# Kernel optimization log

Hardware: AMD Instinct MI355X
Metric: run time of the kernel (lower is better)

## Reference

```python
import jax, jax.numpy as jnp
import numpy as np

N = 50000   # num_nodes
E = 800000  # num_edges (avg degree 16)
D = 128     # input_dim
H = 128     # hidden_dim
EPS = 1e-5


def _linear_params(key, fan_in, fan_out):
    k1, k2 = jax.random.split(key)
    s = 1.0 / np.sqrt(fan_in)
    W = jax.random.uniform(k1, (fan_in, fan_out), jnp.float32, -s, s)
    b = jax.random.uniform(k2, (fan_out,), jnp.float32, -s, s)
    return W, b


def setup_inputs() -> dict:
    key = jax.random.key(0)
    ks = jax.random.split(key, 10)
    x = jax.random.normal(ks[0], (N, D), jnp.float32)
    edge_index = jax.random.randint(ks[1], (2, E), 0, N)
    edge_weight = jax.random.uniform(ks[2], (E,), jnp.float32)
    W1, b1 = _linear_params(ks[3], D, H)
    W2, b2 = _linear_params(ks[4], H, H)
    W3, b3 = _linear_params(ks[5], H, H)
    Wh, bh = _linear_params(ks[6], H, H)
    Wa, ba = _linear_params(ks[7], H, 1)
    Wz, bz = _linear_params(ks[8], H, 1)
    ones = jnp.ones((H,), jnp.float32)
    zeros = jnp.zeros((H,), jnp.float32)
    return dict(x=x, edge_index=edge_index, edge_weight=edge_weight,
                W1=W1, b1=b1, W2=W2, b2=b2, W3=W3, b3=b3,
                g1=ones, be1=zeros, g2=ones, be2=zeros, g3=ones, be3=zeros,
                Wh=Wh, bh=bh, Wa=Wa, ba=ba, Wz=Wz, bz=bz)


def _batchnorm(h, g, b):
    mu = jnp.mean(h, axis=0)
    var = jnp.mean((h - mu) ** 2, axis=0)  # biased, as torch BN training
    return (h - mu) * jax.lax.rsqrt(var + EPS) * g + b


def reference(x, edge_index, edge_weight,
              W1, b1, W2, b2, W3, b3,
              g1, be1, g2, be2, g3, be3,
              Wh, bh, Wa, ba, Wz, bz):
    row, col = edge_index[0], edge_index[1]
    loop = jnp.arange(N)
    row_f = jnp.concatenate([row, loop])   # sources (with self-loops)
    col_f = jnp.concatenate([col, loop])   # targets
    w_f = jnp.concatenate([edge_weight, jnp.ones((N,), edge_weight.dtype)])
    deg = jax.ops.segment_sum(w_f, col_f, num_segments=N)
    dinv = jnp.where(deg > 0, jax.lax.rsqrt(deg), 0.0)
    norm = dinv[row_f] * w_f * dinv[col_f]  # [E+N]

    def conv(h, W, b):
        hw = h @ W  # [N,H]
        msg = hw[row_f] * norm[:, None]  # gather + scale
        return jax.ops.segment_sum(msg, col_f, num_segments=N) + b  # scatter-add

    h = jax.nn.relu(_batchnorm(conv(x, W1, b1), g1, be1))
    h = jax.nn.relu(_batchnorm(conv(h, W2, b2), g2, be2))
    h = jax.nn.relu(_batchnorm(conv(h, W3, b3), g3, be3))
    # dropout is identity in eval
    h = jax.nn.relu(h @ Wh + bh)
    ace = h[0] @ Wa + ba  # target_indices[0]
    h2 = h[1] @ Wz + bz   # target_indices[1]
    return jnp.concatenate([ace, h2], axis=0)  # [2]
```

## Files before the change

### kernel.cpp

```cpp
#include <hip/hip_runtime.h>


typedef unsigned short u16;
typedef unsigned int u32;
typedef unsigned long long u64;
typedef short bf16x8 __attribute__((ext_vector_type(8)));
typedef float f32x4 __attribute__((ext_vector_type(4)));

#define NREP 64

__device__ inline float bf2f(u16 u) { return __uint_as_float(((u32)u) << 16); }
__device__ inline u16 f2bf(float f) {
  u32 u = __float_as_uint(f);
  return (u16)((u + 0x7FFFu + ((u >> 16) & 1u)) >> 16);
}

__global__ __launch_bounds__(256) void k_zero_cnt(int* cnt, int n) {
  int i = blockIdx.x * 256 + threadIdx.x;
  if (i < n) cnt[i] = 0;
}

__global__ __launch_bounds__(256) void k_count_rank(const int* __restrict__ col,
                                                    int* __restrict__ cnt,
                                                    int* __restrict__ rank, int e) {
  int i = blockIdx.x * 256 + threadIdx.x;
  if (i < e) rank[i] = atomicAdd(&cnt[col[i]], 1);
}

__global__ __launch_bounds__(256) void k_scan1(const int* __restrict__ cnt,
                                               int* __restrict__ ptr,
                                               int* __restrict__ bsum, int n) {
  __shared__ int sh[256];
  int t = threadIdx.x;
  int i = blockIdx.x * 256 + t;
  int v = (i < n) ? cnt[i] : 0;
  sh[t] = v;
  __syncthreads();
  for (int d = 1; d < 256; d <<= 1) {
    int u = (t >= d) ? sh[t - d] : 0;
    __syncthreads();
    sh[t] += u;
    __syncthreads();
  }
  if (i < n) ptr[i] = sh[t] - v;
  if (t == 255) bsum[blockIdx.x] = sh[255];
}

__global__ __launch_bounds__(256) void k_scan2(int* __restrict__ bsum, int nb) {
  __shared__ int sh[256];
  int t = threadIdx.x;
  int v = (t < nb) ? bsum[t] : 0;
  sh[t] = v;
  __syncthreads();
  for (int d = 1; d < 256; d <<= 1) {
    int u = (t >= d) ? sh[t - d] : 0;
    __syncthreads();
    sh[t] += u;
    __syncthreads();
  }
  if (t < nb) bsum[t] = sh[t] - v;
}

__global__ __launch_bounds__(256) void k_scan3(int* __restrict__ ptr,
                                               const int* __restrict__ bsum,
                                               int n, int e) {
  int i = blockIdx.x * 256 + threadIdx.x;
  if (i < n) ptr[i] += bsum[blockIdx.x];
  if (i == 0) ptr[n] = e;
}

__global__ __launch_bounds__(256) void k_fill(const int* __restrict__ row,
                                              const int* __restrict__ col,
                                              const float* __restrict__ w,
                                              const int* __restrict__ ptr,
                                              const int* __restrict__ rank,
                                              int2* __restrict__ emeta, int e) {
  int i = blockIdx.x * 256 + threadIdx.x;
  if (i < e) {
    int pos = ptr[col[i]] + rank[i];
    emeta[pos] = make_int2(row[i] << 8, __float_as_int(w[i]));
  }
}

__global__ __launch_bounds__(256) void k_deg_dinv(const int* __restrict__ ptr,
                                                  const int2* __restrict__ emeta,
                                                  float* __restrict__ dinv, int n) {
  int i = blockIdx.x * 256 + threadIdx.x;
  if (i >= n) return;
  int j = ptr[i], end = ptr[i + 1];
  float d = 1.0f;
  for (; j < end; ++j) d += __int_as_float(emeta[j].y);
  dinv[i] = rsqrtf(d);
}

__global__ __launch_bounds__(256) void k_coef(const int* __restrict__ ptr,
                                              int2* __restrict__ emeta,
                                              const float* __restrict__ dinv, int n) {
  int i = blockIdx.x * 256 + threadIdx.x;
  if (i >= n) return;
  float dc = dinv[i];
  int j = ptr[i], end = ptr[i + 1];
  for (; j < end; ++j) {
    int2 m = emeta[j];
    emeta[j] = make_int2(m.x,
        __float_as_int(dinv[m.x >> 8] * __int_as_float(m.y) * dc));
  }
}

__global__ __launch_bounds__(256) void k_wpack(const float* __restrict__ W0,
                                               const float* __restrict__ W1,
                                               const float* __restrict__ W2,
                                               u64* __restrict__ cells) {
  const float* W = (blockIdx.x == 0) ? W0 : (blockIdx.x == 1) ? W1 : W2;
  u64* out = cells + (size_t)blockIdx.x * 4096;
  int t = threadIdx.x;
#pragma unroll
  for (int i = 0; i < 16; ++i) {
    int cell = t + 256 * i;
    int col = cell >> 5;
    int k4 = cell & 31;
    int k = k4 * 4;
    u64 c = (u64)f2bf(W[(size_t)(k + 0) * 128 + col]) |
            ((u64)f2bf(W[(size_t)(k + 1) * 128 + col]) << 16) |
            ((u64)f2bf(W[(size_t)(k + 2) * 128 + col]) << 32) |
            ((u64)f2bf(W[(size_t)(k + 3) * 128 + col]) << 48);
    out[col * 32 + (k4 ^ (col & 15))] = c;
  }
}

__global__ __launch_bounds__(256) void k_gemm(const void* __restrict__ Ain,
                                              int a_is_f32,
                                              const u64* __restrict__ Wc,
                                              u16* __restrict__ C,
                                              const float* __restrict__ ab,
                                              float* __restrict__ Szero,
                                              int n) {
  __shared__ u64 As64[128 * 32];
  __shared__ u64 Ws64[128 * 32];
  __shared__ float absh[256];
  int t = threadIdx.x;
  if (blockIdx.x < 16) {
#pragma unroll
    for (int i = 0; i < 4; ++i)
      Szero[blockIdx.x * 1024 + t + 256 * i] = 0.f;
  }
  {
    const ulonglong2* src = (const ulonglong2*)Wc;
    ulonglong2* dst = (ulonglong2*)Ws64;
#pragma unroll
    for (int i = 0; i < 8; ++i) dst[t + 256 * i] = src[t + 256 * i];
  }
  if (ab) {
    if (t < 128) {
      absh[t] = ab[t];
      absh[128 + t] = ab[128 + t];
    }
  }

  int row0 = blockIdx.x * 128;
  int nr = min(128, n - row0);

  if (a_is_f32) {
    const float4* src = (const float4*)((const float*)Ain + (size_t)row0 * 128);
#pragma unroll
    for (int i = 0; i < 16; ++i) {
      int idx = t + 256 * i;
      int r = idx >> 5;
      int j4 = idx & 31;
      float4 v = (r < nr) ? src[idx] : make_float4(0.f, 0.f, 0.f, 0.f);
      u64 cell = (u64)f2bf(v.x) | ((u64)f2bf(v.y) << 16) |
                 ((u64)f2bf(v.z) << 32) | ((u64)f2bf(v.w) << 48);
      As64[r * 32 + (j4 ^ (r & 15))] = cell;
    }
  } else {
    const u16* A = (const u16*)Ain;
    __syncthreads();
#pragma unroll
    for (int i = 0; i < 8; ++i) {
      int idx = t + 256 * i;
      int r = idx >> 4;
      int c8 = idx & 15;
      u64 lo = 0, hi = 0;
      if (r < nr) {
        const u64* srcq = (const u64*)(A + ((size_t)(row0 + r)) * 128 + c8 * 8);
        lo = srcq[0]; hi = srcq[1];
        if (ab) {
          u64 nl = 0, nh = 0;
#pragma unroll
          for (int j = 0; j < 4; ++j) {
            int c = c8 * 8 + j;
            float f = fmaxf(fmaf(bf2f((u16)(lo >> (16 * j))), absh[c], absh[128 + c]), 0.f);
            nl |= ((u64)f2bf(f)) << (16 * j);
            int c2 = c + 4;
            float f2 = fmaxf(fmaf(bf2f((u16)(hi >> (16 * j))), absh[c2], absh[128 + c2]), 0.f);
            nh |= ((u64)f2bf(f2)) << (16 * j);
          }
          lo = nl; hi = nh;
        }
      }
      As64[r * 32 + ((c8 * 2) ^ (r & 15))] = lo;
      As64[r * 32 + ((c8 * 2 + 1) ^ (r & 15))] = hi;
    }
  }
  __syncthreads();

  int w = t >> 6, l = t & 63;
  int lr = l & 15, kg = l >> 4;
  int rA0 = w * 32 + lr, rA1 = rA0 + 16;
  f32x4 acc[2][8];
#pragma unroll
  for (int m = 0; m < 2; ++m)
#pragma unroll
    for (int nf = 0; nf < 8; ++nf) acc[m][nf] = (f32x4){0.f, 0.f, 0.f, 0.f};

  union Frag { u64 q[2]; bf16x8 v; };
#pragma unroll
  for (int ks = 0; ks < 4; ++ks) {
    int kb = ks * 8 + kg;
    Frag a0, a1;
    a0.q[0] = As64[rA0 * 32 + (kb ^ lr)];
    a0.q[1] = As64[rA0 * 32 + ((kb + 4) ^ lr)];
    a1.q[0] = As64[rA1 * 32 + (kb ^ lr)];
    a1.q[1] = As64[rA1 * 32 + ((kb + 4) ^ lr)];
#pragma unroll
    for (int nf = 0; nf < 8; ++nf) {
      Frag b;
      b.q[0] = Ws64[(nf * 16 + lr) * 32 + (kb ^ lr)];
      b.q[1] = Ws64[(nf * 16 + lr) * 32 + ((kb + 4) ^ lr)];
      acc[0][nf] = __builtin_amdgcn_mfma_f32_16x16x32_bf16(a0.v, b.v, acc[0][nf], 0, 0, 0);
      acc[1][nf] = __builtin_amdgcn_mfma_f32_16x16x32_bf16(a1.v, b.v, acc[1][nf], 0, 0, 0);
    }
  }
#pragma unroll
  for (int m = 0; m < 2; ++m)
#pragma unroll
    for (int nf = 0; nf < 8; ++nf)
#pragma unroll
      for (int j = 0; j < 4; ++j) {
        int gr = row0 + w * 32 + m * 16 + kg * 4 + j;
        if (gr < n) C[(size_t)gr * 128 + nf * 16 + lr] = f2bf(acc[m][nf][j]);
      }
}

__global__ __launch_bounds__(256) void k_gather(const u16* __restrict__ hw,
                                                const int* __restrict__ ptr,
                                                const int2* __restrict__ emeta,
                                                const float* __restrict__ dinv,
                                                u16* __restrict__ out,
                                                float* __restrict__ stats, int n) {
  int w = threadIdx.x >> 6;
  int lane4 = (threadIdx.x & 63) * 4;
  const char* hwb = (const char*)hw;
  float sx = 0.f, sy = 0.f, sxx = 0.f, syy = 0.f;
#pragma unroll
  for (int it = 0; it < 4; ++it) {
    int node = blockIdx.x * 16 + it * 4 + w;
    if (node < n) {
      float di = dinv[node];
      u32 su = *(const u32*)(hwb + ((size_t)node << 8) + lane4);
      float ax0 = __uint_as_float(su << 16) * di * di;
      float ay0 = __uint_as_float(su & 0xFFFF0000u) * di * di;
      float ax1 = 0.f, ay1 = 0.f;
      int j = ptr[node], end = ptr[node + 1];
      for (; j + 3 < end; j += 4) {
        int2 m0 = emeta[j], m1 = emeta[j + 1], m2 = emeta[j + 2], m3 = emeta[j + 3];
        float c0 = __int_as_float(m0.y), c1 = __int_as_float(m1.y);
        float c2 = __int_as_float(m2.y), c3 = __int_as_float(m3.y);
        u32 v0 = *(const u32*)(hwb + m0.x + lane4);
        u32 v1 = *(const u32*)(hwb + m1.x + lane4);
        u32 v2 = *(const u32*)(hwb + m2.x + lane4);
        u32 v3 = *(const u32*)(hwb + m3.x + lane4);
        ax0 = fmaf(__uint_as_float(v0 << 16), c0, ax0);
        ay0 = fmaf(__uint_as_float(v0 & 0xFFFF0000u), c0, ay0);
        ax1 = fmaf(__uint_as_float(v1 << 16), c1, ax1);
        ay1 = fmaf(__uint_as_float(v1 & 0xFFFF0000u), c1, ay1);
        ax0 = fmaf(__uint_as_float(v2 << 16), c2, ax0);
        ay0 = fmaf(__uint_as_float(v2 & 0xFFFF0000u), c2, ay0);
        ax1 = fmaf(__uint_as_float(v3 << 16), c3, ax1);
        ay1 = fmaf(__uint_as_float(v3 & 0xFFFF0000u), c3, ay1);
      }
      for (; j < end; ++j) {
        int2 m0 = emeta[j];
        float c0 = __int_as_float(m0.y);
        u32 v0 = *(const u32*)(hwb + m0.x + lane4);
        ax0 = fmaf(__uint_as_float(v0 << 16), c0, ax0);
        ay0 = fmaf(__uint_as_float(v0 & 0xFFFF0000u), c0, ay0);
      }
      float ax = ax0 + ax1, ay = ay0 + ay1;
      u32 o = (u32)f2bf(ax) | ((u32)f2bf(ay) << 16);
      *(u32*)((char*)out + ((size_t)node << 8) + lane4) = o;
      sx += ax; sy += ay;
      sxx = fmaf(ax, ax, sxx); syy = fmaf(ay, ay, syy);
    }
  }
  __shared__ float4 red[256];
  red[threadIdx.x] = make_float4(sx, sy, sxx, syy);
  __syncthreads();
  if (threadIdx.x < 64) {
    int t = threadIdx.x;
    float4 a = red[t], b = red[t + 64], c = red[t + 128], d = red[t + 192];
    float* S = stats + (blockIdx.x & (NREP - 1)) * 256;
    unsafeAtomicAdd(&S[2 * t],           a.x + b.x + c.x + d.x);
    unsafeAtomicAdd(&S[2 * t + 1],       a.y + b.y + c.y + d.y);
    unsafeAtomicAdd(&S[128 + 2 * t],     a.z + b.z + c.z + d.z);
    unsafeAtomicAdd(&S[128 + 2 * t + 1], a.w + b.w + c.w + d.w);
  }
}

__global__ __launch_bounds__(128) void k_bn_finalize(const float* __restrict__ S,
                                                     const float* __restrict__ g,
                                                     const float* __restrict__ be,
                                                     float* __restrict__ ab, int n) {
  int c = threadIdx.x;
  float s = 0.f, ss = 0.f;
#pragma unroll 8
  for (int r = 0; r < NREP; ++r) {
    s += S[r * 256 + c];
    ss += S[r * 256 + 128 + c];
  }
  float inv_n = 1.0f / (float)n;
  float mu = s * inv_n;
  float var = ss * inv_n - mu * mu;
  float istd = rsqrtf(var + 1e-5f);
  float A = g[c] * istd;
  ab[c] = A;
  ab[128 + c] = fmaf(-mu, A, be[c]);
}

__global__ __launch_bounds__(256) void k_head(const u16* __restrict__ h,
                                              const float* __restrict__ ab,
                                              const float* __restrict__ Wh,
                                              const float* __restrict__ bh,
                                              const float* __restrict__ Wa,
                                              const float* __restrict__ ba,
                                              const float* __restrict__ Wz,
                                              const float* __restrict__ bz,
                                              float* __restrict__ out) {
  __shared__ float hrow[256];
  __shared__ float red[256];
  int t = threadIdx.x;
  {
    int c = t & 127;
    hrow[t] = fmaxf(fmaf(bf2f(h[t]), ab[c], ab[128 + c]), 0.f);
  }
  __syncthreads();
  int j = t & 127, r = t >> 7;
  float acc = bh[j];
  for (int k = 0; k < 128; ++k)
    acc = fmaf(hrow[r * 128 + k], Wh[k * 128 + j], acc);
  float hv = fmaxf(acc, 0.f);
  float wv = (r == 0) ? Wa[j] : Wz[j];
  red[t] = hv * wv;
  __syncthreads();
  for (int s = 64; s >= 1; s >>= 1) {
    if (j < s) red[t] += red[t + s];
    __syncthreads();
  }
  if (t == 0) out[0] = red[0] + ba[0];
  if (t == 128) out[1] = red[128] + bz[0];
}

extern "C" void kernel_launch(void* const* d_in, const int* in_sizes, int n_in,
                              void* d_out, int out_size, void* d_ws, size_t ws_size,
                              hipStream_t stream) {
  const float* x  = (const float*)d_in[0];
  const int*   ei = (const int*)d_in[1];
  const float* ew = (const float*)d_in[2];
  const float* W[3]  = {(const float*)d_in[3], (const float*)d_in[5], (const float*)d_in[7]};
  const float* g[3]  = {(const float*)d_in[9],  (const float*)d_in[11], (const float*)d_in[13]};
  const float* be[3] = {(const float*)d_in[10], (const float*)d_in[12], (const float*)d_in[14]};
  const float* Wh = (const float*)d_in[15];
  const float* bh = (const float*)d_in[16];
  const float* Wa = (const float*)d_in[17];
  const float* ba = (const float*)d_in[18];
  const float* Wz = (const float*)d_in[19];
  const float* bz = (const float*)d_in[20];

  const int n = in_sizes[0] / 128;
  const int e = in_sizes[1] / 2;
  const int* row = ei;
  const int* col = ei + e;

  u16*   hw_b   = (u16*)d_ws;
  u16*   hbuf_b = hw_b + (size_t)n * 128;
  float* dinv   = (float*)(hbuf_b + (size_t)n * 128);
  float* stats3 = dinv + n;
  float* ab     = stats3 + 3 * NREP * 256;
  u64*   wcells = (u64*)(ab + 3 * 256);
  int*   cnt    = (int*)(wcells + 3 * 4096);
  int*   ptr    = cnt + n;
  int*   bsum   = ptr + n + 1;
  int*   rank   = bsum + 256;
  uintptr_t pm  = ((uintptr_t)(rank + e) + 15) & ~(uintptr_t)15;
  int2*  emeta  = (int2*)pm;

  const int nb_n = (n + 255) / 256;
  const int nb_e = (e + 255) / 256;

  k_zero_cnt<<<nb_n, 256, 0, stream>>>(cnt, n);
  k_count_rank<<<nb_e, 256, 0, stream>>>(col, cnt, rank, e);
  k_scan1<<<nb_n, 256, 0, stream>>>(cnt, ptr, bsum, n);
  k_scan2<<<1, 256, 0, stream>>>(bsum, nb_n);
  k_scan3<<<nb_n, 256, 0, stream>>>(ptr, bsum, n, e);
  k_fill<<<nb_e, 256, 0, stream>>>(row, col, ew, ptr, rank, emeta, e);
  k_deg_dinv<<<nb_n, 256, 0, stream>>>(ptr, emeta, dinv, n);
  k_coef<<<nb_n, 256, 0, stream>>>(ptr, emeta, dinv, n);
  k_wpack<<<3, 256, 0, stream>>>(W[0], W[1], W[2], wcells);

  for (int l = 0; l < 3; ++l) {
    const void* hin = (l == 0) ? (const void*)x : (const void*)hbuf_b;
    const float* abp = (l == 0) ? nullptr : (ab + (l - 1) * 256);
    k_gemm<<<(n + 127) / 128, 256, 0, stream>>>(hin, (l == 0) ? 1 : 0,
                                                wcells + (size_t)l * 4096,
                                                hw_b, abp,
                                                stats3 + l * NREP * 256, n);
    k_gather<<<(n + 15) / 16, 256, 0, stream>>>(hw_b, ptr, emeta, dinv, hbuf_b,
                                                stats3 + l * NREP * 256, n);
    k_bn_finalize<<<1, 128, 0, stream>>>(stats3 + l * NREP * 256, g[l], be[l],
                                         ab + l * 256, n);
  }
  k_head<<<1, 256, 0, stream>>>(hbuf_b, ab + 2 * 256, Wh, bh, Wa, ba, Wz, bz,
                                (float*)d_out);
}
```

Baseline: 385.5 us.

## Split gather across column slices with edge-parallel lanes and packed 32-bit edge metadata

Edge metadata is compacted into a 32-bit word holding a 16-bit source index and a bf16 coefficient. The gather kernel is split into 8 column slices per node tile, with 8 lane groups each processing a different edge and combining the partial sums through shuffles. This aims to expose more memory-level parallelism and shrink metadata traffic. In exchange, the metadata is re-read per slice, the coefficient precision drops to bf16, and node indices are limited to 16 bits.

```diff
diff --git a/kernel.cpp b/kernel.cpp
--- a/kernel.cpp
+++ b/kernel.cpp
@@ -78,7 +78,7 @@
   int i = blockIdx.x * 256 + threadIdx.x;
   if (i < e) {
     int pos = ptr[col[i]] + rank[i];
-    emeta[pos] = make_int2(row[i] << 8, __float_as_int(w[i]));
+    emeta[pos] = make_int2(row[i], __float_as_int(w[i]));
   }
 }
 
@@ -94,16 +94,17 @@
 }
 
 __global__ __launch_bounds__(256) void k_coef(const int* __restrict__ ptr,
-                                              int2* __restrict__ emeta,
-                                              const float* __restrict__ dinv, int n) {
+                                              const int2* __restrict__ emeta,
+                                              const float* __restrict__ dinv,
+                                              u32* __restrict__ epack, int n) {
   int i = blockIdx.x * 256 + threadIdx.x;
   if (i >= n) return;
   float dc = dinv[i];
   int j = ptr[i], end = ptr[i + 1];
   for (; j < end; ++j) {
     int2 m = emeta[j];
-    emeta[j] = make_int2(m.x,
-        __float_as_int(dinv[m.x >> 8] * __int_as_float(m.y) * dc));
+    float c = dinv[m.x] * __int_as_float(m.y) * dc;
+    epack[j] = ((u32)m.x << 16) | (u32)f2bf(c);
   }
 }
 
@@ -244,66 +245,62 @@
 
 __global__ __launch_bounds__(256) void k_gather(const u16* __restrict__ hw,
                                                 const int* __restrict__ ptr,
-                                                const int2* __restrict__ emeta,
+                                                const u32* __restrict__ epack,
                                                 const float* __restrict__ dinv,
                                                 u16* __restrict__ out,
                                                 float* __restrict__ stats, int n) {
+  int slice = blockIdx.x & 7;
+  int tile = blockIdx.x >> 3;
   int w = threadIdx.x >> 6;
-  int lane4 = (threadIdx.x & 63) * 4;
+  int lane = threadIdx.x & 63;
+  int es = lane >> 3;
+  int cu = lane & 7;
+  int colb = slice * 32 + cu * 4;
   const char* hwb = (const char*)hw;
   float sx = 0.f, sy = 0.f, sxx = 0.f, syy = 0.f;
 #pragma unroll
   for (int it = 0; it < 4; ++it) {
-    int node = blockIdx.x * 16 + it * 4 + w;
+    int node = tile * 16 + it * 4 + w;
     if (node < n) {
       float di = dinv[node];
-      u32 su = *(const u32*)(hwb + ((size_t)node << 8) + lane4);
-      float ax0 = __uint_as_float(su << 16) * di * di;
-      float ay0 = __uint_as_float(su & 0xFFFF0000u) * di * di;
-      float ax1 = 0.f, ay1 = 0.f;
-      int j = ptr[node], end = ptr[node + 1];
-      for (; j + 3 < end; j += 4) {
-        int2 m0 = emeta[j], m1 = emeta[j + 1], m2 = emeta[j + 2], m3 = emeta[j + 3];
-        float c0 = __int_as_float(m0.y), c1 = __int_as_float(m1.y);
-        float c2 = __int_as_float(m2.y), c3 = __int_as_float(m3.y);
-        u32 v0 = *(const u32*)(hwb + m0.x + lane4);
-        u32 v1 = *(const u32*)(hwb + m1.x + lane4);
-        u32 v2 = *(const u32*)(hwb + m2.x + lane4);
-        u32 v3 = *(const u32*)(hwb + m3.x + lane4);
-        ax0 = fmaf(__uint_as_float(v0 << 16), c0, ax0);
-        ay0 = fmaf(__uint_as_float(v0 & 0xFFFF0000u), c0, ay0);
-        ax1 = fmaf(__uint_as_float(v1 << 16), c1, ax1);
-        ay1 = fmaf(__uint_as_float(v1 & 0xFFFF0000u), c1, ay1);
-        ax0 = fmaf(__uint_as_float(v2 << 16), c2, ax0);
-        ay0 = fmaf(__uint_as_float(v2 & 0xFFFF0000u), c2, ay0);
-        ax1 = fmaf(__uint_as_float(v3 << 16), c3, ax1);
-        ay1 = fmaf(__uint_as_float(v3 & 0xFFFF0000u), c3, ay1);
+      u32 su = *(const u32*)(hwb + ((size_t)node << 8) + colb);
+      float ax = 0.f, ay = 0.f;
+      if (es == 0) {
+        ax = __uint_as_float(su << 16) * di * di;
+        ay = __uint_as_float(su & 0xFFFF0000u) * di * di;
       }
-      for (; j < end; ++j) {
-        int2 m0 = emeta[j];
-        float c0 = __int_as_float(m0.y);
-        u32 v0 = *(const u32*)(hwb + m0.x + lane4);
-        ax0 = fmaf(__uint_as_float(v0 << 16), c0, ax0);
-        ay0 = fmaf(__uint_as_float(v0 & 0xFFFF0000u), c0, ay0);
+      int end = ptr[node + 1];
+      for (int j = ptr[node] + es; j < end; j += 8) {
+        u32 m = __builtin_nontemporal_load(epack + j);
+        float c = __uint_as_float(m << 16);
+        u32 v = *(const u32*)(hwb + ((m & 0xFFFF0000u) >> 8) + colb);
+        ax = fmaf(__uint_as_float(v << 16), c, ax);
+        ay = fmaf(__uint_as_float(v & 0xFFFF0000u), c, ay);
       }
-      float ax = ax0 + ax1, ay = ay0 + ay1;
-      u32 o = (u32)f2bf(ax) | ((u32)f2bf(ay) << 16);
-      *(u32*)((char*)out + ((size_t)node << 8) + lane4) = o;
+      ax += __shfl_xor(ax, 8);  ay += __shfl_xor(ay, 8);
+      ax += __shfl_xor(ax, 16); ay += __shfl_xor(ay, 16);
+      ax += __shfl_xor(ax, 32); ay += __shfl_xor(ay, 32);
+      if (es == 0) {
+        u32 o = (u32)f2bf(ax) | ((u32)f2bf(ay) << 16);
+        __builtin_nontemporal_store(o,
+            (u32*)((char*)out + ((size_t)node << 8) + colb));
+      }
       sx += ax; sy += ay;
       sxx = fmaf(ax, ax, sxx); syy = fmaf(ay, ay, syy);
     }
   }
-  __shared__ float4 red[256];
-  red[threadIdx.x] = make_float4(sx, sy, sxx, syy);
-  __syncthreads();
-  if (threadIdx.x < 64) {
+  __shared__ float4 red[32];
+  if (es == 0) red[w * 8 + cu] = make_float4(sx, sy, sxx, syy);
+  __syncthreads();
+  if (threadIdx.x < 8) {
     int t = threadIdx.x;
-    float4 a = red[t], b = red[t + 64], c = red[t + 128], d = red[t + 192];
-    float* S = stats + (blockIdx.x & (NREP - 1)) * 256;
-    unsafeAtomicAdd(&S[2 * t],           a.x + b.x + c.x + d.x);
-    unsafeAtomicAdd(&S[2 * t + 1],       a.y + b.y + c.y + d.y);
-    unsafeAtomicAdd(&S[128 + 2 * t],     a.z + b.z + c.z + d.z);
-    unsafeAtomicAdd(&S[128 + 2 * t + 1], a.w + b.w + c.w + d.w);
+    float4 a = red[t], b = red[8 + t], c4 = red[16 + t], d = red[24 + t];
+    float* S = stats + (tile & (NREP - 1)) * 256;
+    int c0 = (slice * 8 + t) * 2;
+    unsafeAtomicAdd(&S[c0],           a.x + b.x + c4.x + d.x);
+    unsafeAtomicAdd(&S[c0 + 1],       a.y + b.y + c4.y + d.y);
+    unsafeAtomicAdd(&S[128 + c0],     a.z + b.z + c4.z + d.z);
+    unsafeAtomicAdd(&S[128 + c0 + 1], a.w + b.w + c4.w + d.w);
   }
 }
 
@@ -391,7 +388,8 @@
   int*   ptr    = cnt + n;
   int*   bsum   = ptr + n + 1;
   int*   rank   = bsum + 256;
-  uintptr_t pm  = ((uintptr_t)(rank + e) + 15) & ~(uintptr_t)15;
+  u32*   epack  = (u32*)(rank + e);
+  uintptr_t pm  = ((uintptr_t)(epack + e) + 15) & ~(uintptr_t)15;
   int2*  emeta  = (int2*)pm;
 
   const int nb_n = (n + 255) / 256;
@@ -404,9 +402,10 @@
   k_scan3<<<nb_n, 256, 0, stream>>>(ptr, bsum, n, e);
   k_fill<<<nb_e, 256, 0, stream>>>(row, col, ew, ptr, rank, emeta, e);
   k_deg_dinv<<<nb_n, 256, 0, stream>>>(ptr, emeta, dinv, n);
-  k_coef<<<nb_n, 256, 0, stream>>>(ptr, emeta, dinv, n);
+  k_coef<<<nb_n, 256, 0, stream>>>(ptr, emeta, dinv, epack, n);
   k_wpack<<<3, 256, 0, stream>>>(W[0], W[1], W[2], wcells);
 
+  const int ntile = (n + 15) / 16;
   for (int l = 0; l < 3; ++l) {
     const void* hin = (l == 0) ? (const void*)x : (const void*)hbuf_b;
     const float* abp = (l == 0) ? nullptr : (ab + (l - 1) * 256);
@@ -414,8 +413,8 @@
                                                 wcells + (size_t)l * 4096,
                                                 hw_b, abp,
                                                 stats3 + l * NREP * 256, n);
-    k_gather<<<(n + 15) / 16, 256, 0, stream>>>(hw_b, ptr, emeta, dinv, hbuf_b,
-                                                stats3 + l * NREP * 256, n);
+    k_gather<<<ntile * 8, 256, 0, stream>>>(hw_b, ptr, epack, dinv, hbuf_b,
+                                            stats3 + l * NREP * 256, n);
     k_bn_finalize<<<1, 128, 0, stream>>>(stats3 + l * NREP * 256, g[l], be[l],
                                          ab + l * 256, n);
   }
```

After: 787.4 us. +104.2%, slower.
